# Performance work log

Measured on AMD Instinct MI355X. Metric: run time of the kernel, lower is better.

## Reference

```python
import jax, jax.numpy as jnp
import numpy as np

B, S, T, D, H = 2, 2048, 2048, 512, 8
HD = D // H
CLAMP = 1e9


def _padding_cross_mask(key):
    # emulate cross_mask(): valid prefixes for src and tgt sequences
    k1, k2 = jax.random.split(key)
    src_len = jax.random.randint(k1, (B,), S // 2, S + 1)  # [B]
    tgt_len = jax.random.randint(k2, (B,), T // 2, T + 1)  # [B]
    src_valid = jnp.arange(S)[None, :] < src_len[:, None]  # [B,S]
    tgt_valid = jnp.arange(T)[None, :] < tgt_len[:, None]  # [B,T]
    m = tgt_valid[:, :, None] & src_valid[:, None, :]      # [B,T,S]
    return m[:, None, :, :]                                 # [B,1,T,S]


def setup_inputs() -> dict:
    key = jax.random.key(0)
    ks = jax.random.split(key, 10)
    sc = 0.02
    return {
        "x": jax.random.normal(ks[0], (B, S, D), jnp.float32),
        "y": jax.random.normal(ks[1], (B, T, D), jnp.float32),
        "mask": _padding_cross_mask(ks[2]),
        "kv_w": jax.random.normal(ks[3], (D, 2 * D), jnp.float32) * sc,
        "kv_b": jax.random.normal(ks[4], (2 * D,), jnp.float32) * sc,
        "q_w": jax.random.normal(ks[5], (D, D), jnp.float32) * sc,
        "q_b": jax.random.normal(ks[6], (D,), jnp.float32) * sc,
        "o_w": jax.random.normal(ks[7], (D, D), jnp.float32) * sc,
        "o_b": jax.random.normal(ks[8], (D,), jnp.float32) * sc,
    }


def reference(x, y, mask, kv_w, kv_b, q_w, q_b, o_w, o_b):
    b, t, d = y.shape
    s = x.shape[1]
    kv = x @ kv_w + kv_b                               # [B,S,2D]
    q = y @ q_w + q_b                                  # [B,T,D]
    kv = kv.reshape(b, s, H, 2 * HD).transpose(0, 2, 1, 3)  # [B,H,S,2hd]
    q = q.reshape(b, t, H, HD).transpose(0, 2, 1, 3)        # [B,H,T,hd]
    k, v = kv[..., :HD], kv[..., HD:]
    scores = jnp.einsum("bhtd,bhsd->bhts", q, k) / jnp.sqrt(jnp.float32(HD))
    scores = jnp.where(mask, scores, -jnp.inf)
    scores = jnp.clip(scores, -CLAMP, CLAMP)
    attn = jax.nn.softmax(scores, axis=-1)             # [B,H,T,S]
    vals = jnp.einsum("bhts,bhsd->bhtd", attn, v)
    vals = vals.transpose(0, 2, 1, 3).reshape(b, t, d)
    return vals @ o_w + o_b
```

## Files before the change

### kernel.cpp

```cpp
#include <hip/hip_runtime.h>
#include <hip/hip_bf16.h>
#include <stdint.h>

#define BN 2
#define SL 2048
#define TL 2048
#define DD 512
#define HN 8
#define HDIM 64
#define NSPLIT 2
#define NCHUNK ((SL / NSPLIT) / 64)
#define QSCALE 0.1803368801111f
#define MFIX 12.0f

typedef __attribute__((ext_vector_type(8))) short bf16x8;
typedef __attribute__((ext_vector_type(4))) float f32x4;

static __device__ __forceinline__ unsigned short f2bf(float f) {
    union { float f; unsigned int u; } c; c.f = f;
    unsigned int u = c.u;
    unsigned int r = (u + 0x7fffu + ((u >> 16) & 1u)) >> 16;
    return (unsigned short)r;
}

static __device__ __forceinline__ void gload_lds16(const void* g, void* l) {
    __builtin_amdgcn_global_load_lds(
        (const __attribute__((address_space(1))) unsigned int*)g,
        (__attribute__((address_space(3))) unsigned int*)l, 16, 0, 0);
}

__global__ __launch_bounds__(256) void prep_kernel(
    const float* __restrict__ x, const float* __restrict__ y,
    const float* __restrict__ kv_w, const float* __restrict__ q_w,
    const float* __restrict__ o_w, const void* __restrict__ mask,
    unsigned short* __restrict__ xb, unsigned short* __restrict__ yb,
    unsigned short* __restrict__ kvwT, unsigned short* __restrict__ qwT,
    unsigned short* __restrict__ owT, int* __restrict__ lens,
    float* __restrict__ vmean)
{
    __shared__ unsigned short lds[64][80];
    __shared__ int kind_sh;
    __shared__ int lpart[4];
    int bx = blockIdx.x;
    int tid = threadIdx.x;
    if (bx < 2048) {
        const float* src = (bx < 1024) ? x : y;
        unsigned short* dst = (bx < 1024) ? xb : yb;
        long long i = ((long long)(bx & 1023) * 256 + tid) * 8;
        float4 v0 = *(const float4*)&src[i];
        float4 v1 = *(const float4*)&src[i + 4];
        unsigned long long p0 =
            (unsigned long long)f2bf(v0.x) | ((unsigned long long)f2bf(v0.y) << 16) |
            ((unsigned long long)f2bf(v0.z) << 32) | ((unsigned long long)f2bf(v0.w) << 48);
        unsigned long long p1 =
            (unsigned long long)f2bf(v1.x) | ((unsigned long long)f2bf(v1.y) << 16) |
            ((unsigned long long)f2bf(v1.z) << 32) | ((unsigned long long)f2bf(v1.w) << 48);
        *(unsigned long long*)&dst[i] = p0;
        *(unsigned long long*)&dst[i + 4] = p1;
        return;
    }
    if (bx >= 2308) {
        float4 z = {0.f, 0.f, 0.f, 0.f};
        ((float4*)vmean)[tid] = z;
        return;
    }
    if (bx >= 2304) {
        int blk = bx - 2304;
        int b = blk >> 1, is_tgt = blk & 1;
        if (tid == 0) {
            unsigned int v = *(const unsigned int*)mask;
            int kind = 0;
            if (v == 0x01010101u) kind = 1;
            else if (v == 0x3f800000u) kind = 2;
            else if (v == 0x3f803f80u) kind = 3;
            kind_sh = kind;
        }
        __syncthreads();
        int kind = kind_sh;
        int lane = tid & 63, wid = tid >> 6;
        int cnt = 0;
        for (int i = tid; i < (is_tgt ? TL : SL); i += 256) {
            long long idx = is_tgt ? ((long long)(b * TL + i)) * SL
                                   : ((long long)(b * TL + 0)) * SL + i;
            bool bit;
            if (kind == 0)      bit = ((const int*)mask)[idx] != 0;
            else if (kind == 1) bit = ((const unsigned char*)mask)[idx] != 0;
            else if (kind == 2) bit = ((const float*)mask)[idx] != 0.0f;
            else                bit = ((const unsigned short*)mask)[idx] != 0;
            cnt += bit ? 1 : 0;
        }
        #pragma unroll
        for (int off = 32; off >= 1; off >>= 1) cnt += __shfl_xor(cnt, off, 64);
        if (lane == 0) lpart[wid] = cnt;
        __syncthreads();
        if (tid == 0)
            lens[is_tgt * 2 + b] = lpart[0] + lpart[1] + lpart[2] + lpart[3];
        return;
    }
    const float* W; unsigned short* Wt; int N, tb;
    if (bx < 2176)      { W = kv_w; Wt = kvwT; N = 1024; tb = bx - 2048; }
    else if (bx < 2240) { W = q_w;  Wt = qwT;  N = 512;  tb = bx - 2176; }
    else                { W = o_w;  Wt = owT;  N = 512;  tb = bx - 2240; }
    int nblk = N / 64;
    int n0 = (tb % nblk) * 64, k0 = (tb / nblk) * 64;
    #pragma unroll
    for (int i = 0; i < 4; ++i) {
        int fi = tid + i * 256;
        int kl = fi >> 4;
        int nl = (fi & 15) * 4;
        float4 v = *(const float4*)&W[(long long)(k0 + kl) * N + n0 + nl];
        lds[nl + 0][kl] = f2bf(v.x);
        lds[nl + 1][kl] = f2bf(v.y);
        lds[nl + 2][kl] = f2bf(v.z);
        lds[nl + 3][kl] = f2bf(v.w);
    }
    __syncthreads();
    #pragma unroll
    for (int i = 0; i < 2; ++i) {
        int fi = tid + i * 256;
        int nl = fi >> 3;
        int kl = (fi & 7) * 8;
        *(bf16x8*)&Wt[(long long)(n0 + nl) * 512 + k0 + kl] = *(const bf16x8*)&lds[nl][kl];
    }
}

static __device__ __forceinline__ void mainloop_64x128(
    const unsigned short* __restrict__ Ab, const unsigned short* __restrict__ Bt,
    int m0, int n0, int tid,
    unsigned short* Alds,
    unsigned short* Blds,
    f32x4 (&acc)[2][4])
{
    int lane = tid & 63, wid = tid >> 6;
    int wr = wid >> 1, wc = wid & 1;
    int lr = lane & 15, lg = lane >> 4;
    int rl = lane >> 2;
    int sc = (lane & 3) ^ ((rl >> 1) & 3);

    auto stage = [&](int buf, int kt) {
        #pragma unroll
        for (int j = 0; j < 3; ++j) {
            int seg = wid * 3 + j;
            if (seg < 4) {
                int row = seg * 16 + rl;
                gload_lds16(&Ab[((long long)(m0 + row)) * 512 + kt * 32 + sc * 8],
                            (char*)(Alds + buf * 2048) + seg * 1024);
            } else {
                int s2 = seg - 4;
                int row = s2 * 16 + rl;
                gload_lds16(&Bt[((long long)(n0 + row)) * 512 + kt * 32 + sc * 8],
                            (char*)(Blds + buf * 4096) + s2 * 1024);
            }
        }
    };
    auto frag = [&](const unsigned short* base, int row) -> bf16x8 {
        int slot = lg ^ ((row >> 1) & 3);
        return *(const bf16x8*)((const char*)base + row * 64 + slot * 16);
    };

    stage(0, 0);
    for (int kt = 0; kt < 16; ++kt) {
        int buf = kt & 1;
        if (kt + 1 < 16) {
            stage(buf ^ 1, kt + 1);
            asm volatile("s_waitcnt vmcnt(3)" ::: "memory");
        } else {
            asm volatile("s_waitcnt vmcnt(0)" ::: "memory");
        }
        __syncthreads();
        bf16x8 bfr[4];
        #pragma unroll
        for (int ni = 0; ni < 4; ++ni)
            bfr[ni] = frag(Blds + buf * 4096, wc * 64 + ni * 16 + lr);
        #pragma unroll
        for (int mi = 0; mi < 2; ++mi) {
            bf16x8 afr = frag(Alds + buf * 2048, wr * 32 + mi * 16 + lr);
            #pragma unroll
            for (int ni = 0; ni < 4; ++ni)
                acc[mi][ni] = __builtin_amdgcn_mfma_f32_16x16x32_bf16(
                                  afr, bfr[ni], acc[mi][ni], 0, 0, 0);
        }
        __syncthreads();
    }
}

__global__ __launch_bounds__(256) void gemm_kvq(
    const unsigned short* __restrict__ xb, const unsigned short* __restrict__ yb,
    const unsigned short* __restrict__ kvwT, const unsigned short* __restrict__ qwT,
    const float* __restrict__ kv_b, const float* __restrict__ q_b,
    const int* __restrict__ lens,
    unsigned short* __restrict__ Kbuf, unsigned short* __restrict__ Vtbuf,
    unsigned short* __restrict__ Qbuf, float* __restrict__ vmean)
{
    __shared__ __align__(16) unsigned short Alds[2][64 * 32];
    __shared__ __align__(16) unsigned short Blds[2][128 * 32];
    bool isq = blockIdx.x >= 8;
    int m0 = blockIdx.y * 64;
    if (isq && (m0 & 2047) >= lens[2 + (m0 >> 11)]) return;
    const unsigned short* Ab = isq ? yb : xb;
    const unsigned short* Bt = isq ? qwT : kvwT;
    const float* bias = isq ? q_b : kv_b;
    int n0 = (isq ? (blockIdx.x - 8) : blockIdx.x) * 128;
    int tid = threadIdx.x;
    int lane = tid & 63, wid = tid >> 6;
    int wr = wid >> 1, wc = wid & 1;
    int lr = lane & 15, lg = lane >> 4;

    f32x4 acc[2][4] = {};
    mainloop_64x128(Ab, Bt, m0, n0, tid, &Alds[0][0], &Blds[0][0], acc);

    float vsum[4] = {0.f, 0.f, 0.f, 0.f};
    #pragma unroll
    for (int mi = 0; mi < 2; ++mi)
    #pragma unroll
    for (int ni = 0; ni < 4; ++ni) {
        int n = n0 + wc * 64 + ni * 16 + lr;
        int mbase = m0 + wr * 32 + mi * 16 + lg * 4;
        float bv = bias[n];
        int b = mbase >> 11;
        int s = mbase & 2047;
        if (!isq) {
            int h = n >> 7, j = n & 127;
            if (j < HDIM) {
                long long base = (((long long)(b * HN + h)) * SL + s) * HDIM + j;
                #pragma unroll
                for (int r = 0; r < 4; ++r)
                    Kbuf[base + (long long)r * HDIM] = f2bf(acc[mi][ni][r] + bv);
            } else {
                int d = j - HDIM;
                long long base = (((long long)(b * HN + h)) * HDIM + d) * SL + s;
                unsigned long long p = 0;
                #pragma unroll
                for (int r = 0; r < 4; ++r)
                    p |= (unsigned long long)f2bf(acc[mi][ni][r] + bv) << (16 * r);
                *(unsigned long long*)&Vtbuf[base] = p;
                vsum[ni] += ((acc[mi][ni][0] + bv) + (acc[mi][ni][1] + bv)) +
                            ((acc[mi][ni][2] + bv) + (acc[mi][ni][3] + bv));
            }
        } else {
            int h = n >> 6, j = n & 63;
            long long base = (((long long)(b * HN + h)) * TL + s) * HDIM + j;
            #pragma unroll
            for (int r = 0; r < 4; ++r)
                Qbuf[base + (long long)r * HDIM] = f2bf((acc[mi][ni][r] + bv) * QSCALE);
        }
    }
    if (!isq && wc == 1) {
        int bh = (m0 >> 11) * HN + (n0 >> 7);
        #pragma unroll
        for (int ni = 0; ni < 4; ++ni) {
            float v = vsum[ni];
            v += __shfl_xor(v, 16, 64);
            v += __shfl_xor(v, 32, 64);
            if (lg == 0)
                atomicAdd(&vmean[bh * HDIM + ni * 16 + lr], v * (1.0f / SL));
        }
    }
}

__global__ __launch_bounds__(256) void gemm_out(
    const unsigned short* __restrict__ Ab, const unsigned short* __restrict__ Bt,
    const float* __restrict__ bias, float* __restrict__ outF)
{
    __shared__ __align__(16) unsigned short Alds[2][64 * 32];
    __shared__ __align__(16) unsigned short Blds[2][128 * 32];
    const int N = 512;
    int n0 = blockIdx.x * 128;
    int m0 = blockIdx.y * 64;
    int tid = threadIdx.x;
    int lane = tid & 63, wid = tid >> 6;
    int wr = wid >> 1, wc = wid & 1;
    int lr = lane & 15, lg = lane >> 4;

    f32x4 acc[2][4] = {};
    mainloop_64x128(Ab, Bt, m0, n0, tid, &Alds[0][0], &Blds[0][0], acc);

    #pragma unroll
    for (int mi = 0; mi < 2; ++mi)
    #pragma unroll
    for (int ni = 0; ni < 4; ++ni) {
        int n = n0 + wc * 64 + ni * 16 + lr;
        int mbase = m0 + wr * 32 + mi * 16 + lg * 4;
        float bv = bias[n];
        #pragma unroll
        for (int r = 0; r < 4; ++r)
            outF[(long long)(mbase + r) * N + n] = acc[mi][ni][r] + bv;
    }
}

__global__ __launch_bounds__(256) void attn_kernel(
    const unsigned short* __restrict__ Q,
    const unsigned short* __restrict__ K,
    const unsigned short* __restrict__ Vt,
    const int* __restrict__ lens,
    float* __restrict__ pml,
    float* __restrict__ pacc)
{
    __shared__ unsigned short Kt[2][4096];
    __shared__ unsigned short Vl[2][4096];
    __shared__ unsigned int P32[4][16][32];
    int idx = blockIdx.x;
    int gid = (idx & 7) * 128 + (idx >> 3);
    int t0 = (gid & 31) * 64;
    int bhsp = gid >> 5;
    int bh = bhsp >> 1;
    int sp = bhsp & 1;
    int b = bh >> 3;
    int tid = threadIdx.x;
    int lane = tid & 63, wid = tid >> 6;
    int tcol = lane & 15, lg = lane >> 4;
    int t0w = t0 + wid * 16;
    int src_len = lens[b];
    int tgt_len = lens[2 + b];
    if (t0 >= tgt_len) return;
    int sbase = sp * (SL / NSPLIT);

    int nch = (src_len - sbase + 63) >> 6;
    if (nch > NCHUNK) nch = NCHUNK;
    if (nch <= 0) {
        #pragma unroll
        for (int dc = 0; dc < 4; ++dc)
            #pragma unroll
            for (int r = 0; r < 4; ++r) {
                long long rowidx = (long long)bh * TL + t0w + lg * 4 + r;
                pacc[(rowidx * NSPLIT + sp) * 64 + dc * 16 + tcol] = 0.0f;
            }
        if (lg == 0) {
            long long rowidx = (long long)bh * TL + t0w + tcol;
            pml[rowidx * NSPLIT + sp] = 0.0f;
        }
        return;
    }

    const unsigned short* Qb = Q + ((long long)bh * TL) * HDIM;
    const unsigned short* Kb = K + ((long long)bh * SL) * HDIM;
    const unsigned short* Vb = Vt + ((long long)bh * HDIM) * SL;

    bf16x8 qf0 = *(const bf16x8*)&Qb[(t0w + tcol) * HDIM + lg * 8];
    bf16x8 qf1 = *(const bf16x8*)&Qb[(t0w + tcol) * HDIM + 32 + lg * 8];
    asm volatile("" : "+v"(qf0), "+v"(qf1));

    int sub = lane >> 3;
    int scol = (lane & 7) ^ sub;
    auto stage = [&](int buf, int s0) {
        #pragma unroll
        for (int j = 0; j < 2; ++j) {
            int g = wid * 2 + j;
            int row = g * 8 + sub;
            gload_lds16(&Kb[(s0 + row) * HDIM + scol * 8],
                        (char*)&Kt[buf][0] + g * 1024);
            gload_lds16(&Vb[(long long)row * SL + s0 + scol * 8],
                        (char*)&Vl[buf][0] + g * 1024);
        }
    };

    f32x4 accv[4] = {};
    float l_run = 0.0f;
    int pswz = (tcol & 7) << 2;

    stage(0, sbase);

    for (int sc2 = 0; sc2 < nch; ++sc2) {
        int s0 = sbase + sc2 * 64;
        asm volatile("s_waitcnt vmcnt(0)" ::: "memory");
        __syncthreads();
        if (sc2 + 1 < nch) stage((sc2 + 1) & 1, s0 + 64);
        const char* Kl = (const char*)&Kt[sc2 & 1][0];
        const char* Vlb = (const char*)&Vl[sc2 & 1][0];

        float sv[4][4];
        __builtin_amdgcn_s_setprio(1);
        #pragma unroll
        for (int st = 0; st < 4; ++st) {
            int krow = st * 16 + tcol;
            int swz = (krow & 7) << 4;
            bf16x8 kf0 = *(const bf16x8*)(Kl + krow * 128 + ((lg << 4) ^ swz));
            bf16x8 kf1 = *(const bf16x8*)(Kl + krow * 128 + (((lg + 4) << 4) ^ swz));
            f32x4 sa = {};
            sa = __builtin_amdgcn_mfma_f32_16x16x32_bf16(kf0, qf0, sa, 0, 0, 0);
            sa = __builtin_amdgcn_mfma_f32_16x16x32_bf16(kf1, qf1, sa, 0, 0, 0);
            #pragma unroll
            for (int r = 0; r < 4; ++r) sv[st][r] = sa[r];
        }
        __builtin_amdgcn_s_setprio(0);
        if (s0 + 64 > src_len) {
            #pragma unroll
            for (int st = 0; st < 4; ++st)
                #pragma unroll
                for (int r = 0; r < 4; ++r) {
                    int s = s0 + st * 16 + lg * 4 + r;
                    if (s >= src_len) sv[st][r] = -1e30f;
                }
        }
        float ps[4];
        #pragma unroll
        for (int st = 0; st < 4; ++st) {
            float p0 = __builtin_amdgcn_exp2f(sv[st][0] - MFIX);
            float p1 = __builtin_amdgcn_exp2f(sv[st][1] - MFIX);
            float p2 = __builtin_amdgcn_exp2f(sv[st][2] - MFIX);
            float p3 = __builtin_amdgcn_exp2f(sv[st][3] - MFIX);
            ps[st] = (p0 + p1) + (p2 + p3);
            unsigned int w0, w1;
            asm("v_cvt_pk_bf16_f32 %0, %1, %2" : "=v"(w0) : "v"(p0), "v"(p1));
            asm("v_cvt_pk_bf16_f32 %0, %1, %2" : "=v"(w1) : "v"(p2), "v"(p3));
            int wsw = (st * 8 + lg * 2) ^ pswz;
            *(unsigned long long*)&P32[wid][tcol][wsw] =
                (unsigned long long)w0 | ((unsigned long long)w1 << 32);
        }
        float psum = (ps[0] + ps[1]) + (ps[2] + ps[3]);
        psum += __shfl_xor(psum, 16, 64);
        psum += __shfl_xor(psum, 32, 64);
        l_run += psum;
        asm volatile("s_waitcnt lgkmcnt(0)" ::: "memory");
        __builtin_amdgcn_sched_barrier(0);
        __builtin_amdgcn_s_setprio(1);
        #pragma unroll
        for (int c = 0; c < 2; ++c) {
            bf16x8 pf = *(const bf16x8*)&P32[wid][tcol][(c * 16 + lg * 4) ^ pswz];
            #pragma unroll
            for (int dc = 0; dc < 4; ++dc) {
                int vrow = dc * 16 + tcol;
                bf16x8 vf = *(const bf16x8*)(Vlb + vrow * 128 +
                                             ((((c * 4 + lg) << 4)) ^ ((vrow & 7) << 4)));
                accv[dc] = __builtin_amdgcn_mfma_f32_16x16x32_bf16(pf, vf, accv[dc], 0, 0, 0);
            }
        }
        __builtin_amdgcn_s_setprio(0);
    }

    #pragma unroll
    for (int dc = 0; dc < 4; ++dc)
        #pragma unroll
        for (int r = 0; r < 4; ++r) {
            long long rowidx = (long long)bh * TL + t0w + lg * 4 + r;
            pacc[(rowidx * NSPLIT + sp) * 64 + dc * 16 + tcol] = accv[dc][r];
        }
    if (lg == 0) {
        long long rowidx = (long long)bh * TL + t0w + tcol;
        pml[rowidx * NSPLIT + sp] = l_run;
    }
}

__global__ __launch_bounds__(256) void combine_kernel(
    const float* __restrict__ pml, const float* __restrict__ pacc,
    const float* __restrict__ vmean, const int* __restrict__ lens,
    unsigned short* __restrict__ valsb)
{
    int lane = threadIdx.x & 63, wid = threadIdx.x >> 6;
    const int rows_total = BN * HN * TL;
    for (int row = blockIdx.x * 4 + wid; row < rows_total; row += gridDim.x * 4) {
        int bh = row >> 11, t = row & 2047;
        int b = bh >> 3, h = bh & 7;
        float o;
        if (t >= lens[2 + b]) {
            o = vmean[bh * HDIM + lane];
        } else {
            float l = pml[row * 2 + 0] + pml[row * 2 + 1];
            float a1 = pacc[((long long)row * 2 + 0) * 64 + lane];
            float a2 = pacc[((long long)row * 2 + 1) * 64 + lane];
            o = (a1 + a2) / l;
        }
        valsb[((long long)(b * TL + t)) * DD + h * HDIM + lane] = f2bf(o);
    }
}

extern "C" void kernel_launch(void* const* d_in, const int* in_sizes, int n_in,
                              void* d_out, int out_size, void* d_ws, size_t ws_size,
                              hipStream_t stream)
{
    const float* x    = (const float*)d_in[0];
    const float* y    = (const float*)d_in[1];
    const void*  mask = d_in[2];
    const float* kv_w = (const float*)d_in[3];
    const float* kv_b = (const float*)d_in[4];
    const float* q_w  = (const float*)d_in[5];
    const float* q_b  = (const float*)d_in[6];
    const float* o_w  = (const float*)d_in[7];
    const float* o_b  = (const float*)d_in[8];
    float* out = (float*)d_out;

    char* ws = (char*)d_ws;
    int* lens = (int*)ws;
    unsigned short* Qbuf  = (unsigned short*)(ws + 256);
    unsigned short* Kbuf  = Qbuf + (size_t)2097152;
    unsigned short* Vtbuf = Kbuf + (size_t)2097152;
    float* pml  = (float*)(Vtbuf + (size_t)2097152);
    float* pacc = pml + (size_t)262144;
    unsigned short* valsb = (unsigned short*)(pacc + (size_t)4194304);
    unsigned short* kvwT = valsb + (size_t)2097152;
    unsigned short* qwT  = kvwT + (size_t)524288;
    unsigned short* owT  = qwT + (size_t)262144;
    float* vmean = (float*)(owT + (size_t)262144);
    unsigned short* xb = (unsigned short*)pacc;
    unsigned short* yb = xb + (size_t)2097152;

    prep_kernel<<<2309, 256, 0, stream>>>(x, y, kv_w, q_w, o_w, mask,
                                          xb, yb, kvwT, qwT, owT, lens, vmean);
    gemm_kvq<<<dim3(12, 64), 256, 0, stream>>>(xb, yb, kvwT, qwT, kv_b, q_b,
                                               lens, Kbuf, Vtbuf, Qbuf, vmean);
    attn_kernel<<<1024, 256, 0, stream>>>(Qbuf, Kbuf, Vtbuf, lens, pml, pacc);
    combine_kernel<<<2048, 256, 0, stream>>>(pml, pacc, vmean, lens, valsb);
    gemm_out<<<dim3(4, 64), 256, 0, stream>>>(valsb, owT, o_b, out);
}
```

Baseline: 77.55 us.

## Fuse split-KV combine into attention via atomic last-block-finishes pattern

Removes the separate combine kernel launch. Each attention block bumps a per-tile atomic counter after writing its partial accumulator and row sum, and the second of the two split blocks merges both partials (or writes the vmean fill for padded rows) straight into the bf16 values buffer. The flags are zeroed in the prep kernel. Separately, the shared GEMM mainloop now waits on all loads and syncs before issuing the next stage, which drops one barrier per iteration but serialises load and compute more. Adds threadfence and atomic overhead in return for one fewer launch and one fewer pass over pacc.

```diff
diff --git a/kernel.cpp b/kernel.cpp
--- a/kernel.cpp
+++ b/kernel.cpp
@@ -36,7 +36,7 @@
     unsigned short* __restrict__ xb, unsigned short* __restrict__ yb,
     unsigned short* __restrict__ kvwT, unsigned short* __restrict__ qwT,
     unsigned short* __restrict__ owT, int* __restrict__ lens,
-    float* __restrict__ vmean)
+    float* __restrict__ vmean, int* __restrict__ flags)
 {
     __shared__ unsigned short lds[64][80];
     __shared__ int kind_sh;
@@ -62,6 +62,7 @@
     if (bx >= 2308) {
         float4 z = {0.f, 0.f, 0.f, 0.f};
         ((float4*)vmean)[tid] = z;
+        ((unsigned long long*)flags)[tid] = 0ull;
         return;
     }
     if (bx >= 2304) {
@@ -161,13 +162,9 @@
     stage(0, 0);
     for (int kt = 0; kt < 16; ++kt) {
         int buf = kt & 1;
-        if (kt + 1 < 16) {
-            stage(buf ^ 1, kt + 1);
-            asm volatile("s_waitcnt vmcnt(3)" ::: "memory");
-        } else {
-            asm volatile("s_waitcnt vmcnt(0)" ::: "memory");
-        }
+        asm volatile("s_waitcnt vmcnt(0)" ::: "memory");
         __syncthreads();
+        if (kt + 1 < 16) stage(buf ^ 1, kt + 1);
         bf16x8 bfr[4];
         #pragma unroll
         for (int ni = 0; ni < 4; ++ni)
@@ -180,7 +177,6 @@
                 acc[mi][ni] = __builtin_amdgcn_mfma_f32_16x16x32_bf16(
                                   afr, bfr[ni], acc[mi][ni], 0, 0, 0);
         }
-        __syncthreads();
     }
 }
 
@@ -294,30 +290,156 @@
     const unsigned short* __restrict__ Vt,
     const int* __restrict__ lens,
     float* __restrict__ pml,
-    float* __restrict__ pacc)
+    float* __restrict__ pacc,
+    const float* __restrict__ vmean,
+    int* __restrict__ flags,
+    unsigned short* __restrict__ valsb)
 {
     __shared__ unsigned short Kt[2][4096];
     __shared__ unsigned short Vl[2][4096];
     __shared__ unsigned int P32[4][16][32];
+    __shared__ int second_sh;
     int idx = blockIdx.x;
     int gid = (idx & 7) * 128 + (idx >> 3);
     int t0 = (gid & 31) * 64;
     int bhsp = gid >> 5;
     int bh = bhsp >> 1;
     int sp = bhsp & 1;
-    int b = bh >> 3;
+    int b = bh >> 3, h = bh & 7;
     int tid = threadIdx.x;
     int lane = tid & 63, wid = tid >> 6;
     int tcol = lane & 15, lg = lane >> 4;
     int t0w = t0 + wid * 16;
     int src_len = lens[b];
     int tgt_len = lens[2 + b];
-    if (t0 >= tgt_len) return;
+    int tile = bh * 32 + (t0 >> 6);
+
+    if (t0 >= tgt_len) {
+        if (tid == 0) second_sh = atomicAdd(&flags[tile], 1);
+        __syncthreads();
+        if (second_sh == 1) {
+            float o = vmean[bh * HDIM + lane];
+            unsigned short ob = f2bf(o);
+            for (int i = 0; i < 16; ++i) {
+                int t = t0 + wid * 16 + i;
+                valsb[((long long)(b * TL + t)) * DD + h * HDIM + lane] = ob;
+            }
+        }
+        return;
+    }
     int sbase = sp * (SL / NSPLIT);
-
     int nch = (src_len - sbase + 63) >> 6;
     if (nch > NCHUNK) nch = NCHUNK;
-    if (nch <= 0) {
+
+    if (nch > 0) {
+        const unsigned short* Qb = Q + ((long long)bh * TL) * HDIM;
+        const unsigned short* Kb = K + ((long long)bh * SL) * HDIM;
+        const unsigned short* Vb = Vt + ((long long)bh * HDIM) * SL;
+
+        bf16x8 qf0 = *(const bf16x8*)&Qb[(t0w + tcol) * HDIM + lg * 8];
+        bf16x8 qf1 = *(const bf16x8*)&Qb[(t0w + tcol) * HDIM + 32 + lg * 8];
+        asm volatile("" : "+v"(qf0), "+v"(qf1));
+
+        int sub = lane >> 3;
+        int scol = (lane & 7) ^ sub;
+        auto stage = [&](int buf, int s0) {
+            #pragma unroll
+            for (int j = 0; j < 2; ++j) {
+                int g = wid * 2 + j;
+                int row = g * 8 + sub;
+                gload_lds16(&Kb[(s0 + row) * HDIM + scol * 8],
+                            (char*)&Kt[buf][0] + g * 1024);
+                gload_lds16(&Vb[(long long)row * SL + s0 + scol * 8],
+                            (char*)&Vl[buf][0] + g * 1024);
+            }
+        };
+
+        f32x4 accv[4] = {};
+        float l_run = 0.0f;
+        int pswz = (tcol & 7) << 2;
+
+        stage(0, sbase);
+
+        for (int sc2 = 0; sc2 < nch; ++sc2) {
+            int s0 = sbase + sc2 * 64;
+            asm volatile("s_waitcnt vmcnt(0)" ::: "memory");
+            __syncthreads();
+            if (sc2 + 1 < nch) stage((sc2 + 1) & 1, s0 + 64);
+            const char* Kl = (const char*)&Kt[sc2 & 1][0];
+            const char* Vlb = (const char*)&Vl[sc2 & 1][0];
+
+            float sv[4][4];
+            __builtin_amdgcn_s_setprio(1);
+            #pragma unroll
+            for (int st = 0; st < 4; ++st) {
+                int krow = st * 16 + tcol;
+                int swz = (krow & 7) << 4;
+                bf16x8 kf0 = *(const bf16x8*)(Kl + krow * 128 + ((lg << 4) ^ swz));
+                bf16x8 kf1 = *(const bf16x8*)(Kl + krow * 128 + (((lg + 4) << 4) ^ swz));
+                f32x4 sa = {};
+                sa = __builtin_amdgcn_mfma_f32_16x16x32_bf16(kf0, qf0, sa, 0, 0, 0);
+                sa = __builtin_amdgcn_mfma_f32_16x16x32_bf16(kf1, qf1, sa, 0, 0, 0);
+                #pragma unroll
+                for (int r = 0; r < 4; ++r) sv[st][r] = sa[r];
+            }
+            __builtin_amdgcn_s_setprio(0);
+            if (s0 + 64 > src_len) {
+                #pragma unroll
+                for (int st = 0; st < 4; ++st)
+                    #pragma unroll
+                    for (int r = 0; r < 4; ++r) {
+                        int s = s0 + st * 16 + lg * 4 + r;
+                        if (s >= src_len) sv[st][r] = -1e30f;
+                    }
+            }
+            float ps[4];
+            #pragma unroll
+            for (int st = 0; st < 4; ++st) {
+                float p0 = __builtin_amdgcn_exp2f(sv[st][0] - MFIX);
+                float p1 = __builtin_amdgcn_exp2f(sv[st][1] - MFIX);
+                float p2 = __builtin_amdgcn_exp2f(sv[st][2] - MFIX);
+                float p3 = __builtin_amdgcn_exp2f(sv[st][3] - MFIX);
+                ps[st] = (p0 + p1) + (p2 + p3);
+                unsigned int w0, w1;
+                asm("v_cvt_pk_bf16_f32 %0, %1, %2" : "=v"(w0) : "v"(p0), "v"(p1));
+                asm("v_cvt_pk_bf16_f32 %0, %1, %2" : "=v"(w1) : "v"(p2), "v"(p3));
+                int wsw = (st * 8 + lg * 2) ^ pswz;
+                *(unsigned long long*)&P32[wid][tcol][wsw] =
+                    (unsigned long long)w0 | ((unsigned long long)w1 << 32);
+            }
+            float psum = (ps[0] + ps[1]) + (ps[2] + ps[3]);
+            psum += __shfl_xor(psum, 16, 64);
+            psum += __shfl_xor(psum, 32, 64);
+            l_run += psum;
+            asm volatile("s_waitcnt lgkmcnt(0)" ::: "memory");
+            __builtin_amdgcn_sched_barrier(0);
+            __builtin_amdgcn_s_setprio(1);
+            #pragma unroll
+            for (int c = 0; c < 2; ++c) {
+                bf16x8 pf = *(const bf16x8*)&P32[wid][tcol][(c * 16 + lg * 4) ^ pswz];
+                #pragma unroll
+                for (int dc = 0; dc < 4; ++dc) {
+                    int vrow = dc * 16 + tcol;
+                    bf16x8 vf = *(const bf16x8*)(Vlb + vrow * 128 +
+                                                 ((((c * 4 + lg) << 4)) ^ ((vrow & 7) << 4)));
+                    accv[dc] = __builtin_amdgcn_mfma_f32_16x16x32_bf16(pf, vf, accv[dc], 0, 0, 0);
+                }
+            }
+            __builtin_amdgcn_s_setprio(0);
+        }
+
+        #pragma unroll
+        for (int dc = 0; dc < 4; ++dc)
+            #pragma unroll
+            for (int r = 0; r < 4; ++r) {
+                long long rowidx = (long long)bh * TL + t0w + lg * 4 + r;
+                pacc[(rowidx * NSPLIT + sp) * 64 + dc * 16 + tcol] = accv[dc][r];
+            }
+        if (lg == 0) {
+            long long rowidx = (long long)bh * TL + t0w + tcol;
+            pml[rowidx * NSPLIT + sp] = l_run;
+        }
+    } else {
         #pragma unroll
         for (int dc = 0; dc < 4; ++dc)
             #pragma unroll
@@ -329,138 +451,29 @@
             long long rowidx = (long long)bh * TL + t0w + tcol;
             pml[rowidx * NSPLIT + sp] = 0.0f;
         }
-        return;
-    }
-
-    const unsigned short* Qb = Q + ((long long)bh * TL) * HDIM;
-    const unsigned short* Kb = K + ((long long)bh * SL) * HDIM;
-    const unsigned short* Vb = Vt + ((long long)bh * HDIM) * SL;
-
-    bf16x8 qf0 = *(const bf16x8*)&Qb[(t0w + tcol) * HDIM + lg * 8];
-    bf16x8 qf1 = *(const bf16x8*)&Qb[(t0w + tcol) * HDIM + 32 + lg * 8];
-    asm volatile("" : "+v"(qf0), "+v"(qf1));
-
-    int sub = lane >> 3;
-    int scol = (lane & 7) ^ sub;
-    auto stage = [&](int buf, int s0) {
-        #pragma unroll
-        for (int j = 0; j < 2; ++j) {
-            int g = wid * 2 + j;
-            int row = g * 8 + sub;
-            gload_lds16(&Kb[(s0 + row) * HDIM + scol * 8],
-                        (char*)&Kt[buf][0] + g * 1024);
-            gload_lds16(&Vb[(long long)row * SL + s0 + scol * 8],
-                        (char*)&Vl[buf][0] + g * 1024);
-        }
-    };
-
-    f32x4 accv[4] = {};
-    float l_run = 0.0f;
-    int pswz = (tcol & 7) << 2;
-
-    stage(0, sbase);
-
-    for (int sc2 = 0; sc2 < nch; ++sc2) {
-        int s0 = sbase + sc2 * 64;
-        asm volatile("s_waitcnt vmcnt(0)" ::: "memory");
-        __syncthreads();
-        if (sc2 + 1 < nch) stage((sc2 + 1) & 1, s0 + 64);
-        const char* Kl = (const char*)&Kt[sc2 & 1][0];
-        const char* Vlb = (const char*)&Vl[sc2 & 1][0];
-
-        float sv[4][4];
-        __builtin_amdgcn_s_setprio(1);
-        #pragma unroll
-        for (int st = 0; st < 4; ++st) {
-            int krow = st * 16 + tcol;
-            int swz = (krow & 7) << 4;
-            bf16x8 kf0 = *(const bf16x8*)(Kl + krow * 128 + ((lg << 4) ^ swz));
-            bf16x8 kf1 = *(const bf16x8*)(Kl + krow * 128 + (((lg + 4) << 4) ^ swz));
-            f32x4 sa = {};
-            sa = __builtin_amdgcn_mfma_f32_16x16x32_bf16(kf0, qf0, sa, 0, 0, 0);
-            sa = __builtin_amdgcn_mfma_f32_16x16x32_bf16(kf1, qf1, sa, 0, 0, 0);
-            #pragma unroll
-            for (int r = 0; r < 4; ++r) sv[st][r] = sa[r];
-        }
-        __builtin_amdgcn_s_setprio(0);
-        if (s0 + 64 > src_len) {
-            #pragma unroll
-            for (int st = 0; st < 4; ++st)
-                #pragma unroll
-                for (int r = 0; r < 4; ++r) {
-                    int s = s0 + st * 16 + lg * 4 + r;
-                    if (s >= src_len) sv[st][r] = -1e30f;
-                }
-        }
-        float ps[4];
-        #pragma unroll
-        for (int st = 0; st < 4; ++st) {
-            float p0 = __builtin_amdgcn_exp2f(sv[st][0] - MFIX);
-            float p1 = __builtin_amdgcn_exp2f(sv[st][1] - MFIX);
-            float p2 = __builtin_amdgcn_exp2f(sv[st][2] - MFIX);
-            float p3 = __builtin_amdgcn_exp2f(sv[st][3] - MFIX);
-            ps[st] = (p0 + p1) + (p2 + p3);
-            unsigned int w0, w1;
-            asm("v_cvt_pk_bf16_f32 %0, %1, %2" : "=v"(w0) : "v"(p0), "v"(p1));
-            asm("v_cvt_pk_bf16_f32 %0, %1, %2" : "=v"(w1) : "v"(p2), "v"(p3));
-            int wsw = (st * 8 + lg * 2) ^ pswz;
-            *(unsigned long long*)&P32[wid][tcol][wsw] =
-                (unsigned long long)w0 | ((unsigned long long)w1 << 32);
-        }
-        float psum = (ps[0] + ps[1]) + (ps[2] + ps[3]);
-        psum += __shfl_xor(psum, 16, 64);
-        psum += __shfl_xor(psum, 32, 64);
-        l_run += psum;
-        asm volatile("s_waitcnt lgkmcnt(0)" ::: "memory");
-        __builtin_amdgcn_sched_barrier(0);
-        __builtin_amdgcn_s_setprio(1);
-        #pragma unroll
-        for (int c = 0; c < 2; ++c) {
-            bf16x8 pf = *(const bf16x8*)&P32[wid][tcol][(c * 16 + lg * 4) ^ pswz];
-            #pragma unroll
-            for (int dc = 0; dc < 4; ++dc) {
-                int vrow = dc * 16 + tcol;
-                bf16x8 vf = *(const bf16x8*)(Vlb + vrow * 128 +
-                                             ((((c * 4 + lg) << 4)) ^ ((vrow & 7) << 4)));
-                accv[dc] = __builtin_amdgcn_mfma_f32_16x16x32_bf16(pf, vf, accv[dc], 0, 0, 0);
-            }
-        }
-        __builtin_amdgcn_s_setprio(0);
-    }
-
-    #pragma unroll
-    for (int dc = 0; dc < 4; ++dc)
-        #pragma unroll
-        for (int r = 0; r < 4; ++r) {
-            long long rowidx = (long long)bh * TL + t0w + lg * 4 + r;
-            pacc[(rowidx * NSPLIT + sp) * 64 + dc * 16 + tcol] = accv[dc][r];
-        }
-    if (lg == 0) {
-        long long rowidx = (long long)bh * TL + t0w + tcol;
-        pml[rowidx * NSPLIT + sp] = l_run;
-    }
-}
-
-__global__ __launch_bounds__(256) void combine_kernel(
-    const float* __restrict__ pml, const float* __restrict__ pacc,
-    const float* __restrict__ vmean, const int* __restrict__ lens,
-    unsigned short* __restrict__ valsb)
-{
-    int lane = threadIdx.x & 63, wid = threadIdx.x >> 6;
-    const int rows_total = BN * HN * TL;
-    for (int row = blockIdx.x * 4 + wid; row < rows_total; row += gridDim.x * 4) {
-        int bh = row >> 11, t = row & 2047;
-        int b = bh >> 3, h = bh & 7;
-        float o;
-        if (t >= lens[2 + b]) {
-            o = vmean[bh * HDIM + lane];
-        } else {
-            float l = pml[row * 2 + 0] + pml[row * 2 + 1];
-            float a1 = pacc[((long long)row * 2 + 0) * 64 + lane];
-            float a2 = pacc[((long long)row * 2 + 1) * 64 + lane];
-            o = (a1 + a2) / l;
-        }
-        valsb[((long long)(b * TL + t)) * DD + h * HDIM + lane] = f2bf(o);
+    }
+
+    __threadfence();
+    __syncthreads();
+    if (tid == 0) second_sh = atomicAdd(&flags[tile], 1);
+    __syncthreads();
+    if (second_sh == 1) {
+        __threadfence();
+        float vm = vmean[bh * HDIM + lane];
+        for (int i = 0; i < 16; ++i) {
+            int t = t0 + wid * 16 + i;
+            long long rowidx = (long long)bh * TL + t;
+            float o;
+            if (t >= tgt_len) {
+                o = vm;
+            } else {
+                float l = pml[rowidx * 2 + 0] + pml[rowidx * 2 + 1];
+                float a1 = pacc[(rowidx * 2 + 0) * 64 + lane];
+                float a2 = pacc[(rowidx * 2 + 1) * 64 + lane];
+                o = (a1 + a2) / l;
+            }
+            valsb[((long long)(b * TL + t)) * DD + h * HDIM + lane] = f2bf(o);
+        }
     }
 }
 
@@ -491,14 +504,16 @@
     unsigned short* qwT  = kvwT + (size_t)524288;
     unsigned short* owT  = qwT + (size_t)262144;
     float* vmean = (float*)(owT + (size_t)262144);
+    int* flags = (int*)(vmean + 1024);
     unsigned short* xb = (unsigned short*)pacc;
     unsigned short* yb = xb + (size_t)2097152;
 
     prep_kernel<<<2309, 256, 0, stream>>>(x, y, kv_w, q_w, o_w, mask,
-                                          xb, yb, kvwT, qwT, owT, lens, vmean);
+                                          xb, yb, kvwT, qwT, owT, lens,
+                                          vmean, flags);
     gemm_kvq<<<dim3(12, 64), 256, 0, stream>>>(xb, yb, kvwT, qwT, kv_b, q_b,
                                                lens, Kbuf, Vtbuf, Qbuf, vmean);
-    attn_kernel<<<1024, 256, 0, stream>>>(Qbuf, Kbuf, Vtbuf, lens, pml, pacc);
-    combine_kernel<<<2048, 256, 0, stream>>>(pml, pacc, vmean, lens, valsb);
+    attn_kernel<<<1024, 256, 0, stream>>>(Qbuf, Kbuf, Vtbuf, lens, pml, pacc,
+                                          vmean, flags, valsb);
     gemm_out<<<dim3(4, 64), 256, 0, stream>>>(valsb, owT, o_b, out);
 }
```

After: 258.5 us. 233% more time.
